# Kernel tuning notes

Hardware: AMD Instinct MI355X
Metric: run time of the kernel (lower is better)

## Reference

```python
import jax, jax.numpy as jnp
import numpy as np

B, T, INPUT_DIM = 4, 2048, 256
D_MODEL = 512                       # hidden_dim // 2
EXPAND = 2
D_INNER = D_MODEL * EXPAND          # 1024
HEADDIM = 128                       # _pick_headdim(1024)
NHEADS = D_INNER // HEADDIM         # 8
DSTATE = 16
DCONV = 4
NLAYERS = 4
CONV_DIM = D_INNER + 2 * DSTATE            # 1056
D_IN_PROJ = 2 * D_INNER + 2 * DSTATE + NHEADS  # 2088
EPS = 1e-5


def _dir_params(key):
    ks = jax.random.split(key, 5)
    return dict(
        in_w=jax.random.normal(ks[0], (NLAYERS, D_IN_PROJ, D_MODEL)) * 0.02,
        conv_w=jax.random.normal(ks[1], (NLAYERS, CONV_DIM, DCONV)) * 0.1,
        conv_b=jnp.zeros((NLAYERS, CONV_DIM)),
        dt_bias=jnp.log(jnp.expm1(jax.random.uniform(ks[2], (NLAYERS, NHEADS), minval=1e-3, maxval=0.1))),
        A_log=jnp.log(jax.random.uniform(ks[3], (NLAYERS, NHEADS), minval=1.0, maxval=16.0)),
        D=jnp.ones((NLAYERS, NHEADS)),
        rms_w=jnp.ones((NLAYERS, D_INNER)),
        out_w=jax.random.normal(ks[4], (NLAYERS, D_MODEL, D_INNER)) * 0.02,
    )


def setup_inputs():
    key = jax.random.key(0)
    kx, ke, kf, kb = jax.random.split(key, 4)
    inp = {
        "x": jax.random.normal(kx, (B, T, INPUT_DIM), dtype=jnp.float32),
        "embed_w": jax.random.normal(ke, (D_MODEL, INPUT_DIM)) * 0.02,
        "embed_b": jnp.zeros((D_MODEL,)),
        "ln1_w": jnp.ones((D_MODEL,)), "ln1_b": jnp.zeros((D_MODEL,)),
        "lnout_w": jnp.ones((2 * D_MODEL,)), "lnout_b": jnp.zeros((2 * D_MODEL,)),
    }
    for tag, p in (("f", _dir_params(kf)), ("b", _dir_params(kb))):
        for k, v in p.items():
            inp[f"{k}_{tag}"] = v
    return inp


def _silu(x):
    return x * jax.nn.sigmoid(x)


def _layernorm(x, w, b):
    m = jnp.mean(x, -1, keepdims=True)
    v = jnp.mean((x - m) ** 2, -1, keepdims=True)
    return (x - m) * jax.lax.rsqrt(v + EPS) * w + b


def _mamba2(h, in_w, conv_w, conv_b, dt_bias, A_log, Dh, rms_w, out_w):
    """One Mamba2 (SSD) block: in_proj -> causal depthwise conv -> selective scan
    -> gated RMSNorm -> out_proj. Sequential scan is math-equivalent to the
    chunked SSD kernel."""
    Bb, Tt, _ = h.shape
    zxbcdt = jnp.einsum('btd,ed->bte', h, in_w)
    z = zxbcdt[..., :D_INNER]
    xBC = zxbcdt[..., D_INNER:D_INNER + CONV_DIM]
    dt = zxbcdt[..., D_INNER + CONV_DIM:]                      # [B,T,H]
    # causal depthwise conv over time (kernel DCONV), then silu
    xc = jax.lax.conv_general_dilated(
        jnp.transpose(xBC, (0, 2, 1)), conv_w[:, None, :], (1,),
        [(DCONV - 1, 0)], feature_group_count=CONV_DIM)
    xBC = _silu(jnp.transpose(xc, (0, 2, 1)) + conv_b)
    xs = xBC[..., :D_INNER].reshape(Bb, Tt, NHEADS, HEADDIM)   # [B,T,H,P]
    Bm = xBC[..., D_INNER:D_INNER + DSTATE]                    # [B,T,N]
    Cm = xBC[..., D_INNER + DSTATE:]                           # [B,T,N]
    dt = jax.nn.softplus(dt + dt_bias)                         # [B,T,H]
    dA = jnp.exp(dt * (-jnp.exp(A_log)))                       # [B,T,H]
    xdt = xs * dt[..., None]                                   # [B,T,H,P]
    tm = lambda a: jnp.moveaxis(a, 1, 0)                       # time-major

    def step(s, inp):
        dA_t, xdt_t, B_t, C_t = inp
        s = dA_t[:, :, None, None] * s + xdt_t[..., None] * B_t[:, None, None, :]
        return s, jnp.einsum('bhpn,bn->bhp', s, C_t)

    s0 = jnp.zeros((Bb, NHEADS, HEADDIM, DSTATE), h.dtype)
    _, ys = jax.lax.scan(step, s0, (tm(dA), tm(xdt), tm(Bm), tm(Cm)))
    y = jnp.moveaxis(ys, 0, 1) + Dh[None, None, :, None] * xs
    y = y.reshape(Bb, Tt, D_INNER)
    g = y * _silu(z)                                           # gated RMSNorm (norm after gate)
    g = g * jax.lax.rsqrt(jnp.mean(g * g, -1, keepdims=True) + EPS) * rms_w
    return jnp.einsum('bti,oi->bto', g, out_w)


def _forward(x, embed_w, embed_b, ln1_w, ln1_b, lnout_w, lnout_b,
             in_w_f, conv_w_f, conv_b_f, dt_bias_f, A_log_f, D_f, rms_w_f, out_w_f,
             in_w_b, conv_w_b, conv_b_b, dt_bias_b, A_log_b, D_b, rms_w_b, out_w_b):
    h = _layernorm(jnp.einsum('bti,oi->bto', x, embed_w) + embed_b, ln1_w, ln1_b)
    h_f, h_b = h, h[:, ::-1]
    for i in range(NLAYERS):
        h_f = _mamba2(h_f, in_w_f[i], conv_w_f[i], conv_b_f[i], dt_bias_f[i],
                      A_log_f[i], D_f[i], rms_w_f[i], out_w_f[i]) + h_f
    for i in range(NLAYERS):
        h_b = _mamba2(h_b, in_w_b[i], conv_w_b[i], conv_b_b[i], dt_bias_b[i],
                      A_log_b[i], D_b[i], rms_w_b[i], out_w_b[i]) + h_b
    out = jnp.concatenate([h_f, h_b[:, ::-1]], axis=-1)        # [B,T,2*D_MODEL]
    return _layernorm(out, lnout_w, lnout_b)


def reference(x, embed_w, embed_b, ln1_w, ln1_b, lnout_w, lnout_b,
              in_w_f, conv_w_f, conv_b_f, dt_bias_f, A_log_f, D_f, rms_w_f, out_w_f,
              in_w_b, conv_w_b, conv_b_b, dt_bias_b, A_log_b, D_b, rms_w_b, out_w_b):
    return _forward(x, embed_w, embed_b, ln1_w, ln1_b, lnout_w, lnout_b,
                    in_w_f, conv_w_f, conv_b_f, dt_bias_f, A_log_f, D_f, rms_w_f, out_w_f,
                    in_w_b, conv_w_b, conv_b_b, dt_bias_b, A_log_b, D_b, rms_w_b, out_w_b)
```

## Files before the change

### kernel.cpp

```cpp
#include <hip/hip_runtime.h>
#include <hip/hip_bf16.h>
#include <math.h>

#define BB 4
#define TT 2048
#define BT 8192
#define DM 512
#define DI 1024
#define NH 8
#define HD 128
#define DS 16
#define CONVD 1056
#define DPROJ 2088
#define NL 4
#define NE 131072

typedef __hip_bfloat16 bf16;
typedef __attribute__((ext_vector_type(8))) short short8;
typedef __attribute__((ext_vector_type(4))) short short4v;
typedef __attribute__((ext_vector_type(4))) float f32x4;

#define AS_G __attribute__((address_space(1)))
#define AS_L __attribute__((address_space(3)))

static __device__ __forceinline__ float b2f_raw(short v){
  union { unsigned u; float f; } c; c.u = ((unsigned)(unsigned short)v) << 16; return c.f;
}
static __device__ __forceinline__ float u32_lo(unsigned u){
  union { unsigned u; float f; } c; c.u = u << 16; return c.f;
}
static __device__ __forceinline__ float u32_hi(unsigned u){
  union { unsigned u; float f; } c; c.u = u & 0xffff0000u; return c.f;
}
static __device__ __forceinline__ unsigned pack_bf16x2(float a, float b){
  unsigned lo = __bfloat16_as_ushort(__float2bfloat16(a));
  unsigned hi = __bfloat16_as_ushort(__float2bfloat16(b));
  return lo | (hi << 16);
}

static __device__ __forceinline__ void red2(float& a, float& b, float* sb){
  #pragma unroll
  for (int o = 32; o; o >>= 1){ a += __shfl_down(a, o); b += __shfl_down(b, o); }
  int w = threadIdx.x >> 6;
  if ((threadIdx.x & 63) == 0){ sb[w] = a; sb[4+w] = b; }
  __syncthreads();
  a = sb[0]+sb[1]+sb[2]+sb[3];
  b = sb[4]+sb[5]+sb[6]+sb[7];
}

__global__ __launch_bounds__(256) void detect_dtype(const void* x, int* flagp){
  __shared__ int cnt;
  if (threadIdx.x == 0) cnt = 0;
  __syncthreads();
  const bf16* p = (const bf16*)x;
  int bad = 0;
  for (int i = threadIdx.x; i < 32768; i += 256){
    float v = __bfloat162float(p[i]);
    if (!isfinite(v) || fabsf(v) > 1e4f) bad++;
  }
  atomicAdd(&cnt, bad);
  __syncthreads();
  if (threadIdx.x == 0) *flagp = (cnt > 100) ? 1 : 0;
}

__global__ __launch_bounds__(256) void convert_in(const void* src, bf16* dst, int n,
                                                  const int* flagp){
  int f = *flagp;
  for (int i = blockIdx.x*256 + threadIdx.x; i < n; i += gridDim.x*256){
    if (f) dst[i] = __float2bfloat16(((const float*)src)[i]);
    else   dst[i] = ((const bf16*)src)[i];
  }
}

template<int OP>
__global__ __launch_bounds__(256,4) void gemm_nt(
    const bf16* __restrict__ A, const bf16* __restrict__ W0, const bf16* __restrict__ W1,
    bf16* C, const bf16* X, float* aux,
    int M, int N, int K, int lda, long sA, long sC)
{
  const int z = blockIdx.z;
  const bf16* Az = A + (long)z * sA;
  const bf16* W = z ? W1 : W0;
  const int m0 = blockIdx.x * 128, n0 = blockIdx.y * 128;
  __shared__ __align__(16) bf16 As[2][128*32];
  __shared__ __align__(16) bf16 Bs[2][128*32];
  const int tid  = threadIdx.x;
  const int lane = tid & 63, wv = tid >> 6;
  const int wmB = (wv >> 1)*64;
  const int wnB = (wv & 1)*64;
  const int quad = lane >> 4, l16 = lane & 15;
  const int srow = lane >> 2;
  const int skb  = (((lane & 3) ^ ((srow >> 1) & 3)) * 16);
  const int rslot = ((quad ^ ((l16 >> 1) & 3)) * 16);

  f32x4 acc[4][4];
  #pragma unroll
  for (int i=0;i<4;i++)
    #pragma unroll
    for (int j=0;j<4;j++) acc[i][j] = (f32x4){0.f,0.f,0.f,0.f};

  auto stage = [&](int k0, int buf){
    #pragma unroll
    for (int is = 0; is < 2; ++is){
      int r = is*64 + wv*16 + srow;
      const char* gA = (const char*)(Az + (long)(m0 + r)*lda + k0) + skb;
      char* lA = (char*)(&As[buf][0]) + (long)(is*64 + wv*16)*64;
      __builtin_amdgcn_global_load_lds((const AS_G void*)gA, (AS_L void*)lA, 16, 0, 0);
    }
    #pragma unroll
    for (int is = 0; is < 2; ++is){
      int r = is*64 + wv*16 + srow;
      int rn = n0 + r; rn = rn < N ? rn : N-1;
      const char* gB = (const char*)(W + (long)rn*K + k0) + skb;
      char* lB = (char*)(&Bs[buf][0]) + (long)(is*64 + wv*16)*64;
      __builtin_amdgcn_global_load_lds((const AS_G void*)gB, (AS_L void*)lB, 16, 0, 0);
    }
  };
  auto compute = [&](int buf){
    short8 af[4], bfr[4];
    #pragma unroll
    for (int mi=0;mi<4;mi++)
      af[mi]  = *(const short8*)((const char*)&As[buf][0] + (long)(wmB+mi*16+l16)*64 + rslot);
    #pragma unroll
    for (int ni=0;ni<4;ni++)
      bfr[ni] = *(const short8*)((const char*)&Bs[buf][0] + (long)(wnB+ni*16+l16)*64 + rslot);
    #pragma unroll
    for (int mi=0;mi<4;mi++)
      #pragma unroll
      for (int ni=0;ni<4;ni++)
        acc[mi][ni] = __builtin_amdgcn_mfma_f32_16x16x32_bf16(af[mi], bfr[ni], acc[mi][ni], 0, 0, 0);
  };

  stage(0, 0);
  __syncthreads();
  for (int k0 = 0; k0 < K; k0 += 64){
    if (k0 + 32 < K) stage(k0 + 32, 1);
    compute(0);
    __syncthreads();
    if (k0 + 64 < K) stage(k0 + 64, 0);
    compute(1);
    __syncthreads();
  }

  bf16* Cz = C + (long)z * sC;
  const bf16* Xz = (OP==2) ? (X + (long)z * sC) : X;
  #pragma unroll
  for (int mi=0;mi<4;mi++){
    #pragma unroll
    for (int ni=0;ni<4;ni++){
      #pragma unroll
      for (int r=0;r<4;r++){
        int row = m0 + wmB + mi*16 + quad*4 + r;
        int col = n0 + wnB + ni*16 + l16;
        if (col < N){
          float v = acc[mi][ni][r];
          if (OP==1) v += __bfloat162float(X[col]);
          if (OP==2) v += __bfloat162float(Xz[(long)row*N + col]);
          Cz[(long)row*N + col] = __float2bfloat16(v);
          if (OP==3 && col >= DPROJ-8)
            aux[(long)z*BT*8 + (long)row*8 + (col-(DPROJ-8))] = v;
        }
      }
    }
  }
}

__global__ __launch_bounds__(256) void embed_ln(const bf16* __restrict__ hp,
    const bf16* __restrict__ w, const bf16* __restrict__ bb, bf16* __restrict__ h)
{
  __shared__ float sb[8];
  int bt = blockIdx.x; int b = bt >> 11, t = bt & 2047;
  const bf16* r = hp + (long)bt*DM;
  int c0 = threadIdx.x, c1 = threadIdx.x + 256;
  float v0 = __bfloat162float(r[c0]);
  float v1 = __bfloat162float(r[c1]);
  float s = v0+v1, ss = v0*v0+v1*v1;
  red2(s, ss, sb);
  float m = s / DM;
  float var = ss / DM - m*m;
  float rs = rsqrtf(fmaxf(var, 0.f) + 1e-5f);
  float a0 = (v0-m)*rs*__bfloat162float(w[c0]) + __bfloat162float(bb[c0]);
  float a1 = (v1-m)*rs*__bfloat162float(w[c1]) + __bfloat162float(bb[c1]);
  bf16* o0 = h + (long)bt*DM;
  bf16* o1 = h + ((long)BT + (long)b*TT + (TT-1-t)) * DM;
  o0[c0] = __float2bfloat16(a0); o0[c1] = __float2bfloat16(a1);
  o1[c0] = __float2bfloat16(a0); o1[c1] = __float2bfloat16(a1);
}

__global__ __launch_bounds__(256) void conv_silu(const bf16* __restrict__ zx,
    const bf16* __restrict__ cw0, const bf16* __restrict__ cw1,
    const bf16* __restrict__ cb0, const bf16* __restrict__ cb1,
    bf16* __restrict__ xbc)
{
  int bt = blockIdx.x, dir = blockIdx.y;
  int t = bt & 2047;
  const bf16* cw = dir ? cw1 : cw0;
  const bf16* cb = dir ? cb1 : cb0;
  const bf16* zr = zx + ((long)dir*BT + bt)*DPROJ + DI;
  bf16* orow = xbc + ((long)dir*BT + bt)*CONVD;
  for (int cg = threadIdx.x; cg < CONVD/4; cg += 256){
    int c = cg*4;
    short8 w01 = *(const short8*)(cw + c*4);
    short8 w23 = *(const short8*)(cw + c*4 + 8);
    short4v bi = *(const short4v*)(cb + c);
    float acc[4];
    #pragma unroll
    for (int k=0;k<4;k++) acc[k] = b2f_raw(bi[k]);
    #pragma unroll
    for (int j=0;j<4;j++){
      if (t - 3 + j >= 0){
        short4v xv = *(const short4v*)(zr + (long)(j-3)*DPROJ + c);
        acc[0] = fmaf(b2f_raw(w01[j]),   b2f_raw(xv[0]), acc[0]);
        acc[1] = fmaf(b2f_raw(w01[4+j]), b2f_raw(xv[1]), acc[1]);
        acc[2] = fmaf(b2f_raw(w23[j]),   b2f_raw(xv[2]), acc[2]);
        acc[3] = fmaf(b2f_raw(w23[4+j]), b2f_raw(xv[3]), acc[3]);
      }
    }
    short4v ov;
    #pragma unroll
    for (int k=0;k<4;k++){
      float sg = 1.f / (1.f + expf(-acc[k]));
      ov[k] = (short)__bfloat16_as_ushort(__float2bfloat16(acc[k] * sg));
    }
    *(short4v*)(orow + c) = ov;
  }
}

__global__ __launch_bounds__(256) void dt_kernel(const float* __restrict__ draw,
    const bf16* __restrict__ db0, const bf16* __restrict__ db1,
    const bf16* __restrict__ al0, const bf16* __restrict__ al1,
    float2* __restrict__ dadt)
{
  int idx = blockIdx.x*256 + threadIdx.x;
  int dir = idx >> 16, r = idx & 65535;
  int bt = r >> 3, h = r & 7;
  int b = bt >> 11, t = bt & 2047;
  float x = draw[idx] + __bfloat162float((dir?db1:db0)[h]);
  float sp = (x > 20.f) ? x : log1pf(expf(x));
  float a = expf(-expf(__bfloat162float((dir?al1:al0)[h])) * sp);
  long o = (((long)dir*BB + b)*NH + h)*TT + t;
  float2 v; v.x = a; v.y = sp;
  dadt[o] = v;
}

#define CLG_LOAD(G, T0) do{ \
  _Pragma("unroll") \
  for (int _i=0;_i<4;_i++){ \
    const bf16* _rr = xr + (long)((T0)+_i)*CONVD; \
    G##x[_i]  = *(const unsigned*)(_rr + xoff); \
    G##B0[_i] = *(const short8*)(_rr + DI); \
    G##B1[_i] = *(const short8*)(_rr + DI + 8); \
    G##d[_i]  = ddr[(T0)+_i]; \
  } }while(0)

#define CLG_STEP(G) do{ \
  _Pragma("unroll") \
  for (int _i=0;_i<4;_i++){ \
    float _da = G##d[_i].x, _dt = G##d[_i].y; \
    float _x0 = u32_lo(G##x[_i]), _x1 = u32_hi(G##x[_i]); \
    float _xd0 = _x0*_dt, _xd1 = _x1*_dt; \
    _Pragma("unroll") \
    for (int _n=0;_n<8;_n++){ \
      float _b = b2f_raw(G##B0[_i][_n]); \
      s0[_n] = fmaf(_da, s0[_n], _xd0*_b); \
      s1[_n] = fmaf(_da, s1[_n], _xd1*_b); \
      float _b2 = b2f_raw(G##B1[_i][_n]); \
      s0[8+_n] = fmaf(_da, s0[8+_n], _xd0*_b2); \
      s1[8+_n] = fmaf(_da, s1[8+_n], _xd1*_b2); \
    } \
    pacc *= _da; \
  } }while(0)

__global__ __launch_bounds__(256,1) void chunk_local(const bf16* __restrict__ xbc,
    const float2* __restrict__ dadt, float* __restrict__ SC, float* __restrict__ Pc,
    int cl, int nch)
{
  int c = blockIdx.x;
  int dbh = blockIdx.y*4 + (threadIdx.x >> 6);
  int lane = threadIdx.x & 63;
  int dir = dbh >> 5, b = (dbh >> 3) & 3, h = dbh & 7;
  const bf16* xr = xbc + ((long)dir*BT + (long)b*TT) * CONVD;
  const float2* ddr = dadt + (long)dbh*TT;
  const int xoff = h*HD + lane*2;
  float s0[16], s1[16];
  #pragma unroll
  for (int n=0;n<16;n++){ s0[n]=0.f; s1[n]=0.f; }
  float pacc = 1.f;
  const int c0 = c*cl;

  unsigned Ax[4], Bx[4]; short8 AB0[4], AB1[4], BB0[4], BB1[4]; float2 Ad[4], Bd[4];
  CLG_LOAD(A, c0);
  for (int t0 = c0; t0 < c0+cl; t0 += 8){
    CLG_LOAD(B, t0+4);
    CLG_STEP(A);
    if (t0+8 < c0+cl) CLG_LOAD(A, t0+8);
    CLG_STEP(B);
  }
  float* sc = SC + (long)c*NE + (long)dbh*2048 + lane*32;
  #pragma unroll
  for (int n=0;n<16;n++){ sc[n] = s0[n]; sc[16+n] = s1[n]; }
  if (lane == 0) Pc[dbh*nch + c] = pacc;
}

template<int NCH>
__global__ __launch_bounds__(256) void chunk_combine(float* __restrict__ SC,
    const float* __restrict__ Pc)
{
  int e = blockIdx.x*256 + threadIdx.x;
  int dbh = e >> 11;
  float s = 0.f;
  #pragma unroll
  for (int c=0;c<NCH;c++){
    float tmp = SC[(long)c*NE + e];
    SC[(long)c*NE + e] = s;
    s = Pc[dbh*NCH + c]*s + tmp;
  }
}

__global__ __launch_bounds__(512,2) void chunk_apply_gate(
    const bf16* __restrict__ xbc, bf16* __restrict__ zx,
    const float2* __restrict__ dadt, const float* __restrict__ SC,
    const bf16* __restrict__ D0, const bf16* __restrict__ D1,
    const bf16* __restrict__ rw0, const bf16* __restrict__ rw1, int cl)
{
  __shared__ float sb[8][4];
  int c = blockIdx.x;
  int db = blockIdx.y;
  int dir = db >> 2, b = db & 3;
  int h = threadIdx.x >> 6;
  int lane = threadIdx.x & 63;
  int dbh = dir*32 + b*8 + h;
  const bf16* xr = xbc + ((long)dir*BT + (long)b*TT) * CONVD;
  bf16* zrow = zx + ((long)dir*BT + (long)b*TT) * DPROJ;
  const float2* ddr = dadt + (long)dbh*TT;
  const int xoff = h*HD + lane*2;
  float Dv = __bfloat162float(dir ? D1[h] : D0[h]);
  const bf16* rw = dir ? rw1 : rw0;
  float rwl = __bfloat162float(rw[xoff]);
  float rwh = __bfloat162float(rw[xoff+1]);
  const float* sc = SC + (long)c*NE + (long)dbh*2048 + lane*32;
  float s0[16], s1[16];
  #pragma unroll
  for (int n=0;n<16;n++){ s0[n] = sc[n]; s1[n] = sc[16+n]; }
  const int c0 = c*cl;

  for (int t0 = c0; t0 < c0+cl; t0 += 4){
    float gl[4], gh[4], sum2[4];
    #pragma unroll
    for (int i=0;i<4;i++){
      const bf16* rr = xr + (long)(t0+i)*CONVD;
      unsigned xv = *(const unsigned*)(rr + xoff);
      short8 B0 = *(const short8*)(rr + DI);
      short8 B1 = *(const short8*)(rr + DI + 8);
      short8 C0 = *(const short8*)(rr + DI + DS);
      short8 C1 = *(const short8*)(rr + DI + DS + 8);
      unsigned zv = *(const unsigned*)(zrow + (long)(t0+i)*DPROJ + xoff);
      float2 dd = ddr[t0+i];
      float da = dd.x, dt = dd.y;
      float x0 = u32_lo(xv), x1 = u32_hi(xv);
      float xd0 = x0*dt, xd1 = x1*dt;
      float a0 = 0.f, a1 = 0.f;
      #pragma unroll
      for (int n=0;n<8;n++){
        float bb0 = b2f_raw(B0[n]), cc0 = b2f_raw(C0[n]);
        s0[n] = fmaf(da, s0[n], xd0*bb0);
        s1[n] = fmaf(da, s1[n], xd1*bb0);
        a0 = fmaf(s0[n], cc0, a0);
        a1 = fmaf(s1[n], cc0, a1);
        float bb1 = b2f_raw(B1[n]), cc1 = b2f_raw(C1[n]);
        s0[8+n] = fmaf(da, s0[8+n], xd0*bb1);
        s1[8+n] = fmaf(da, s1[8+n], xd1*bb1);
        a0 = fmaf(s0[8+n], cc1, a0);
        a1 = fmaf(s1[8+n], cc1, a1);
      }
      float y0 = a0 + Dv*x0, y1 = a1 + Dv*x1;
      float z0 = u32_lo(zv), z1 = u32_hi(zv);
      float g0 = y0 * z0 * (1.f/(1.f+expf(-z0)));
      float g1 = y1 * z1 * (1.f/(1.f+expf(-z1)));
      gl[i] = g0; gh[i] = g1;
      sum2[i] = g0*g0 + g1*g1;
    }
    #pragma unroll
    for (int o=32;o;o>>=1){
      #pragma unroll
      for (int i=0;i<4;i++) sum2[i] += __shfl_down(sum2[i], o);
    }
    if (lane == 0){
      #pragma unroll
      for (int i=0;i<4;i++) sb[h][i] = sum2[i];
    }
    __syncthreads();
    float scl[4];
    #pragma unroll
    for (int i=0;i<4;i++){
      float tot = 0.f;
      #pragma unroll
      for (int w=0;w<8;w++) tot += sb[w][i];
      scl[i] = rsqrtf(tot*(1.f/DI) + 1e-5f);
    }
    __syncthreads();
    #pragma unroll
    for (int i=0;i<4;i++)
      *(unsigned*)(zrow + (long)(t0+i)*DPROJ + xoff) =
          pack_bf16x2(gl[i]*scl[i]*rwl, gh[i]*scl[i]*rwh);
  }
}

__global__ __launch_bounds__(256) void final_ln(const bf16* __restrict__ h,
    const bf16* __restrict__ lw, const bf16* __restrict__ lb, void* out,
    int mode, const int* flagp)
{
  __shared__ float sb[8];
  int bt = blockIdx.x; int b = bt >> 11, t = bt & 2047;
  int f32out = mode ? *flagp : 0;
  const bf16* rf = h + (long)bt*DM;
  const bf16* rb = h + ((long)BT + (long)b*TT + (TT-1-t))*DM;
  float v[4], s = 0.f, ss = 0.f;
  #pragma unroll
  for (int i=0;i<4;i++){
    int c = threadIdx.x + i*256;
    v[i] = __bfloat162float(c < DM ? rf[c] : rb[c-DM]);
    s += v[i]; ss += v[i]*v[i];
  }
  red2(s, ss, sb);
  float m = s / (2*DM);
  float var = ss / (2*DM) - m*m;
  float rs = rsqrtf(fmaxf(var, 0.f) + 1e-5f);
  #pragma unroll
  for (int i=0;i<4;i++){
    int c = threadIdx.x + i*256;
    float o = (v[i]-m)*rs*__bfloat162float(lw[c]) + __bfloat162float(lb[c]);
    if (f32out) ((float*)out)[(long)bt*(2*DM) + c] = o;
    else        ((bf16*)out)[(long)bt*(2*DM) + c] = __float2bfloat16(o);
  }
}

extern "C" void kernel_launch(void* const* d_in, const int* in_sizes, int n_in,
                              void* d_out, int out_size, void* d_ws, size_t ws_size,
                              hipStream_t stream)
{
  char* wsp = (char*)d_ws;
  auto take = [&](size_t bytes){ char* p = wsp; wsp += (bytes + 63) & ~(size_t)63; return p; };
  int*   flagp = (int*)  take(4);
  bf16*  h     = (bf16*) take((size_t)2*BT*DM*2);
  bf16*  zx    = (bf16*) take((size_t)2*BT*DPROJ*2);
  bf16*  xbc   = (bf16*) take((size_t)2*BT*CONVD*2);
  float2* dadt = (float2*)take((size_t)2*BB*NH*TT*8);
  float* draw  = (float*)take((size_t)2*BT*NH*4);
  float* Pc    = (float*)take((size_t)64*64*4);
  char* preCanon = wsp;

  static const int cnt[23] = {
    BT*256, DM*256, DM, DM, DM, 2*DM, 2*DM,
    NL*DPROJ*DM, NL*CONVD*4, NL*CONVD, NL*NH, NL*NH, NL*NH, NL*DI, NL*DM*DI,
    NL*DPROJ*DM, NL*CONVD*4, NL*CONVD, NL*NH, NL*NH, NL*NH, NL*DI, NL*DM*DI };
  bf16* canon[23];
  for (int i = 0; i < 23; ++i) canon[i] = (bf16*)take((size_t)cnt[i]*2);
  char* postCanon = wsp;

  const size_t scUnit = (size_t)NE*4;
  size_t usedFull   = (size_t)(postCanon - (char*)d_ws);
  size_t usedDirect = (size_t)(preCanon  - (char*)d_ws);
  int convMode, NCHR; float* SC;
  if      (ws_size >= usedFull + 64*scUnit){ convMode=1; NCHR=64; SC=(float*)postCanon; }
  else if (ws_size >= usedFull + 32*scUnit){ convMode=1; NCHR=32; SC=(float*)postCanon; }
  else if (ws_size >= usedFull + 16*scUnit){ convMode=1; NCHR=16; SC=(float*)postCanon; }
  else {
    convMode = 0;
    if      (ws_size >= usedDirect + 64*scUnit) NCHR=64;
    else if (ws_size >= usedDirect + 32*scUnit) NCHR=32;
    else                                        NCHR=16;
    SC = (float*)preCanon;
  }
  const int CLR = TT / NCHR;

  const bf16* in[23];
  if (convMode){
    detect_dtype<<<1,256,0,stream>>>(d_in[0], flagp);
    for (int i = 0; i < 23; ++i){
      int grid = (cnt[i] + 255)/256; if (grid > 2048) grid = 2048;
      convert_in<<<grid,256,0,stream>>>(d_in[i], canon[i], cnt[i], flagp);
      in[i] = canon[i];
    }
  } else {
    for (int i = 0; i < 23; ++i) in[i] = (const bf16*)d_in[i];
  }

  const bf16* x       = in[0];
  const bf16* embed_w = in[1];
  const bf16* embed_b = in[2];
  const bf16* ln1_w   = in[3];
  const bf16* ln1_b   = in[4];
  const bf16* lnout_w = in[5];
  const bf16* lnout_b = in[6];
  const bf16* in_w[2]   = {in[7],  in[15]};
  const bf16* conv_w[2] = {in[8],  in[16]};
  const bf16* conv_b[2] = {in[9],  in[17]};
  const bf16* dt_b[2]   = {in[10], in[18]};
  const bf16* A_log[2]  = {in[11], in[19]};
  const bf16* Dp[2]     = {in[12], in[20]};
  const bf16* rms_w[2]  = {in[13], in[21]};
  const bf16* out_w[2]  = {in[14], in[22]};

  bf16* hpre = xbc;

  gemm_nt<1><<<dim3(64,4,1),256,0,stream>>>(x, embed_w, embed_w, hpre, embed_b, nullptr,
                                            BT, DM, 256, 256, 0, 0);
  embed_ln<<<dim3(BT),256,0,stream>>>(hpre, ln1_w, ln1_b, h);

  for (int i = 0; i < NL; ++i){
    gemm_nt<3><<<dim3(64,17,2),256,0,stream>>>(h, in_w[0]+(size_t)i*DPROJ*DM, in_w[1]+(size_t)i*DPROJ*DM,
        zx, nullptr, draw, BT, DPROJ, DM, DM, (long)BT*DM, (long)BT*DPROJ);
    conv_silu<<<dim3(BT,2),256,0,stream>>>(zx, conv_w[0]+(size_t)i*CONVD*4, conv_w[1]+(size_t)i*CONVD*4,
        conv_b[0]+(size_t)i*CONVD, conv_b[1]+(size_t)i*CONVD, xbc);
    dt_kernel<<<dim3(512),256,0,stream>>>(draw, dt_b[0]+i*NH, dt_b[1]+i*NH,
        A_log[0]+i*NH, A_log[1]+i*NH, dadt);
    chunk_local<<<dim3(NCHR,16),256,0,stream>>>(xbc, dadt, SC, Pc, CLR, NCHR);
    if      (NCHR == 64) chunk_combine<64><<<dim3(NE/256),256,0,stream>>>(SC, Pc);
    else if (NCHR == 32) chunk_combine<32><<<dim3(NE/256),256,0,stream>>>(SC, Pc);
    else                 chunk_combine<16><<<dim3(NE/256),256,0,stream>>>(SC, Pc);
    chunk_apply_gate<<<dim3(NCHR,8),512,0,stream>>>(xbc, zx, dadt, SC,
        Dp[0]+i*NH, Dp[1]+i*NH, rms_w[0]+(size_t)i*DI, rms_w[1]+(size_t)i*DI, CLR);
    gemm_nt<2><<<dim3(64,4,2),256,0,stream>>>(zx, out_w[0]+(size_t)i*DM*DI, out_w[1]+(size_t)i*DM*DI,
        h, h, nullptr, BT, DM, DI, DPROJ, (long)BT*DPROJ, (long)BT*DM);
  }

  final_ln<<<dim3(BT),256,0,stream>>>(h, lnout_w, lnout_b, d_out, convMode, flagp);
  (void)in_sizes; (void)n_in; (void)out_size;
}
```

Before: 1.224 ms.

## Defer RMSNorm scale to out_proj epilogue, removing per-step block barriers

New measurement: 1.137 ms. 1.08x faster.

```diff
diff --git a/kernel.cpp b/kernel.cpp
--- a/kernel.cpp
+++ b/kernel.cpp
@@ -143,7 +143,7 @@
   }
 
   bf16* Cz = C + (long)z * sC;
-  const bf16* Xz = (OP==2) ? (X + (long)z * sC) : X;
+  const bf16* Xz = (OP==2 || OP==4) ? (X + (long)z * sC) : X;
   #pragma unroll
   for (int mi=0;mi<4;mi++){
     #pragma unroll
@@ -156,6 +156,10 @@
           float v = acc[mi][ni][r];
           if (OP==1) v += __bfloat162float(X[col]);
           if (OP==2) v += __bfloat162float(Xz[(long)row*N + col]);
+          if (OP==4){
+            v *= aux[(long)z*BT + row];
+            v += __bfloat162float(Xz[(long)row*N + col]);
+          }
           Cz[(long)row*N + col] = __float2bfloat16(v);
           if (OP==3 && col >= DPROJ-8)
             aux[(long)z*BT*8 + (long)row*8 + (col-(DPROJ-8))] = v;
@@ -321,9 +325,9 @@
     const bf16* __restrict__ xbc, bf16* __restrict__ zx,
     const float2* __restrict__ dadt, const float* __restrict__ SC,
     const bf16* __restrict__ D0, const bf16* __restrict__ D1,
-    const bf16* __restrict__ rw0, const bf16* __restrict__ rw1, int cl)
-{
-  __shared__ float sb[8][4];
+    const bf16* __restrict__ rw0, const bf16* __restrict__ rw1,
+    float* __restrict__ psum, int cl)
+{
   int c = blockIdx.x;
   int db = blockIdx.y;
   int dir = db >> 2, b = db & 3;
@@ -332,6 +336,7 @@
   int dbh = dir*32 + b*8 + h;
   const bf16* xr = xbc + ((long)dir*BT + (long)b*TT) * CONVD;
   bf16* zrow = zx + ((long)dir*BT + (long)b*TT) * DPROJ;
+  const long rowB = (long)dir*BT + (long)b*TT;
   const float2* ddr = dadt + (long)dbh*TT;
   const int xoff = h*HD + lane*2;
   float Dv = __bfloat162float(dir ? D1[h] : D0[h]);
@@ -377,8 +382,8 @@
       float z0 = u32_lo(zv), z1 = u32_hi(zv);
       float g0 = y0 * z0 * (1.f/(1.f+expf(-z0)));
       float g1 = y1 * z1 * (1.f/(1.f+expf(-z1)));
-      gl[i] = g0; gh[i] = g1;
       sum2[i] = g0*g0 + g1*g1;
+      gl[i] = g0*rwl; gh[i] = g1*rwh;
     }
     #pragma unroll
     for (int o=32;o;o>>=1){
@@ -387,23 +392,22 @@
     }
     if (lane == 0){
       #pragma unroll
-      for (int i=0;i<4;i++) sb[h][i] = sum2[i];
-    }
-    __syncthreads();
-    float scl[4];
-    #pragma unroll
-    for (int i=0;i<4;i++){
-      float tot = 0.f;
-      #pragma unroll
-      for (int w=0;w<8;w++) tot += sb[w][i];
-      scl[i] = rsqrtf(tot*(1.f/DI) + 1e-5f);
-    }
-    __syncthreads();
+      for (int i=0;i<4;i++) psum[(rowB + t0 + i)*8 + h] = sum2[i];
+    }
     #pragma unroll
     for (int i=0;i<4;i++)
-      *(unsigned*)(zrow + (long)(t0+i)*DPROJ + xoff) =
-          pack_bf16x2(gl[i]*scl[i]*rwl, gh[i]*scl[i]*rwh);
-  }
+      *(unsigned*)(zrow + (long)(t0+i)*DPROJ + xoff) = pack_bf16x2(gl[i], gh[i]);
+  }
+}
+
+__global__ __launch_bounds__(256) void rms_scl(const float* __restrict__ psum,
+                                               float* __restrict__ scl)
+{
+  int r = blockIdx.x*256 + threadIdx.x;
+  float s = 0.f;
+  #pragma unroll
+  for (int w=0;w<8;w++) s += psum[(long)r*8 + w];
+  scl[r] = rsqrtf(s*(1.f/DI) + 1e-5f);
 }
 
 __global__ __launch_bounds__(256) void final_ln(const bf16* __restrict__ h,
@@ -448,6 +452,8 @@
   float2* dadt = (float2*)take((size_t)2*BB*NH*TT*8);
   float* draw  = (float*)take((size_t)2*BT*NH*4);
   float* Pc    = (float*)take((size_t)64*64*4);
+  float* psum  = (float*)take((size_t)2*BT*8*4);
+  float* scl   = (float*)take((size_t)2*BT*4);
   char* preCanon = wsp;
 
   static const int cnt[23] = {
@@ -520,9 +526,10 @@
     else if (NCHR == 32) chunk_combine<32><<<dim3(NE/256),256,0,stream>>>(SC, Pc);
     else                 chunk_combine<16><<<dim3(NE/256),256,0,stream>>>(SC, Pc);
     chunk_apply_gate<<<dim3(NCHR,8),512,0,stream>>>(xbc, zx, dadt, SC,
-        Dp[0]+i*NH, Dp[1]+i*NH, rms_w[0]+(size_t)i*DI, rms_w[1]+(size_t)i*DI, CLR);
-    gemm_nt<2><<<dim3(64,4,2),256,0,stream>>>(zx, out_w[0]+(size_t)i*DM*DI, out_w[1]+(size_t)i*DM*DI,
-        h, h, nullptr, BT, DM, DI, DPROJ, (long)BT*DPROJ, (long)BT*DM);
+        Dp[0]+i*NH, Dp[1]+i*NH, rms_w[0]+(size_t)i*DI, rms_w[1]+(size_t)i*DI, psum, CLR);
+    rms_scl<<<dim3(2*BT/256),256,0,stream>>>(psum, scl);
+    gemm_nt<4><<<dim3(64,4,2),256,0,stream>>>(zx, out_w[0]+(size_t)i*DM*DI, out_w[1]+(size_t)i*DM*DI,
+        h, h, scl, BT, DM, DI, DPROJ, (long)BT*DPROJ, (long)BT*DM);
   }
 
   final_ln<<<dim3(BT),256,0,stream>>>(h, lnout_w, lnout_b, d_out, convMode, flagp);
```
